# Performance work log

Hardware: AMD Instinct MI355X
Metric: run time of the kernel (lower is better)

Reference implementation:

```python
import jax, jax.numpy as jnp
import numpy as np

N = 250000   # nodes
E = 500000   # edges
D = 128      # embed_dim
L = 4        # num_layer - 1 conv layers
G = 10000    # graphs in batch
OUT = 128    # output_dim
AV = 120     # atom vocab per feature
BV = 6       # bond vocab per feature
EPS_GN = 1e-6


def setup_inputs() -> dict:
    key = jax.random.key(0)
    ks = jax.random.split(key, 12)
    s = 0.02
    f32 = jnp.float32
    inp = {}
    inp["nfeat"] = jax.random.randint(ks[0], (N, 9), 0, AV)
    inp["efeat"] = jax.random.randint(ks[1], (E, 3), 0, BV)
    inp["src"] = jax.random.randint(ks[2], (E,), 0, N)
    inp["dst"] = jax.random.randint(ks[3], (E,), 0, N)
    inp["graph_ids"] = jnp.arange(N, dtype=jnp.int32) // (N // G)  # 25 nodes/graph
    # learned params
    inp["atom_emb"] = jax.random.normal(ks[4], (9, AV, D), f32) * s
    inp["bond_emb"] = jax.random.normal(ks[5], (L, 3, BV, D), f32) * s
    inp["W1"] = jax.random.normal(ks[6], (L, D, 2 * D), f32) * s
    inp["b1"] = jnp.zeros((L, 2 * D), f32)
    inp["gn1_w"] = jnp.ones((L, 2 * D), f32)
    inp["gn1_b"] = jnp.zeros((L, 2 * D), f32)
    inp["gn1_ms"] = jnp.ones((L, 2 * D), f32)  # GraphNorm mean_scale
    inp["W2"] = jax.random.normal(ks[7], (L, 2 * D, D), f32) * s
    inp["b2"] = jnp.zeros((L, D), f32)
    inp["gn2_w"] = jnp.ones((L, D), f32)
    inp["gn2_b"] = jnp.zeros((L, D), f32)
    inp["gn2_ms"] = jnp.ones((L, D), f32)
    inp["Wp"] = jax.random.normal(ks[8], (D, OUT), f32) * s
    inp["bp"] = jnp.zeros((OUT,), f32)
    return inp


def graph_norm(x, gids, counts, w, b, ms):
    # GraphNorm: x - mean_scale * per-graph mean, / per-graph std, affine
    mean = jax.ops.segment_sum(x, gids, num_segments=G) / counts  # [G, D]
    sub = x - mean[gids] * ms
    var = jax.ops.segment_sum(sub * sub, gids, num_segments=G) / counts
    std = jnp.sqrt(var + EPS_GN)
    return w * sub / std[gids] + b


def reference(nfeat, efeat, src, dst, graph_ids, atom_emb, bond_emb,
              W1, b1, gn1_w, gn1_b, gn1_ms, W2, b2, gn2_w, gn2_b, gn2_ms,
              Wp, bp):
    counts = jax.ops.segment_sum(jnp.ones((N, 1), jnp.float32), graph_ids,
                                 num_segments=G)  # [G,1]
    # AtomEncoder: sum of 9 per-feature embeddings
    h = jnp.sum(atom_emb[jnp.arange(9)[None, :], nfeat], axis=1)  # [N, D]
    eps = jnp.float32(0.0)  # GIN eps buffer, init 0, not learned
    for l in range(L):
        x = h
        # BondEncoder for layer l
        he = jnp.sum(bond_emb[l][jnp.arange(3)[None, :], efeat], axis=1)  # [E, D]
        m = h[src] + he                                   # copy_u + edge add
        agg = jax.ops.segment_sum(m, dst, num_segments=N)  # sum reduce
        rst = (agg + (1.0 + eps) * h) @ W1[l] + b1[l]
        rst = graph_norm(rst, graph_ids, counts, gn1_w[l], gn1_b[l], gn1_ms[l])
        rst = jax.nn.relu(rst) @ W2[l] + b2[l]
        rst = graph_norm(rst, graph_ids, counts, gn2_w[l], gn2_b[l], gn2_ms[l])
        if l != L - 1:
            rst = jax.nn.relu(rst)  # activation for all but last conv layer
        h = rst + x  # residual
    # mean pooling over graphs
    g = jax.ops.segment_sum(h, graph_ids, num_segments=G) / counts  # [G, D]
    # dropout is identity in eval mode
    return g @ Wp + bp
```

## Files before the change

kernel.cpp:

```cpp
#include <hip/hip_runtime.h>
#include <hip/hip_bf16.h>
#include <stdint.h>

#define N_NODES 250000
#define N_EDGES 500000
#define DIM     128
#define D2      256
#define NLAYER  4
#define NGRAPH  10000
#define NPG     25
#define ATOMV   120
#define BONDV   6
#define NBCOMB  216

typedef __attribute__((ext_vector_type(4))) float f32x4;
typedef __attribute__((ext_vector_type(8))) short bf16x8;

__device__ __forceinline__ unsigned short bf16c(float x) {
    union { __hip_bfloat16 b; unsigned short u; } v;
    v.b = __float2bfloat16(x);
    return v.u;
}
__device__ __forceinline__ float bf16_up(unsigned short b) {
    union { float f; unsigned u; } v; v.u = (unsigned)b << 16;
    return v.f;
}
__device__ __forceinline__ f32x4 up4(ushort4 v) {
    f32x4 r;
    r[0] = bf16_up(v.x); r[1] = bf16_up(v.y);
    r[2] = bf16_up(v.z); r[3] = bf16_up(v.w);
    return r;
}

template<int CTRL>
__device__ __forceinline__ float dppadd(float x) {
    return x + __builtin_bit_cast(float,
        __builtin_amdgcn_update_dpp(0, __builtin_bit_cast(int, x),
                                    CTRL, 0xF, 0xF, true));
}
template<int CTRL>
__device__ __forceinline__ void red_step(f32x4& s0, f32x4& q0, f32x4& s1, f32x4& q1) {
#pragma unroll
    for (int j = 0; j < 4; ++j) {
        s0[j] = dppadd<CTRL>(s0[j]);
        q0[j] = dppadd<CTRL>(q0[j]);
        s1[j] = dppadd<CTRL>(s1[j]);
        q1[j] = dppadd<CTRL>(q1[j]);
    }
}
__device__ __forceinline__ void red16(f32x4& s0, f32x4& q0, f32x4& s1, f32x4& q1) {
    red_step<0xB1>(s0, q0, s1, q1);
    red_step<0x4E>(s0, q0, s1, q1);
    red_step<0x124>(s0, q0, s1, q1);
    red_step<0x128>(s0, q0, s1, q1);
}

__global__ void k_atom(const int* __restrict__ nfeat, const float* __restrict__ aemb,
                       unsigned short* __restrict__ h) {
    int t = blockIdx.x * 256 + threadIdx.x;
    int n = t >> 5;
    if (n >= N_NODES) return;
    int q = (t & 31) * 4;
    f32x4 acc = {0.f, 0.f, 0.f, 0.f};
#pragma unroll
    for (int f = 0; f < 9; ++f) {
        int v = nfeat[n * 9 + f];
        acc += *(const f32x4*)(aemb + ((size_t)(f * ATOMV + v) * DIM + q));
    }
    ushort4 hv;
    hv.x = bf16c(acc[0]); hv.y = bf16c(acc[1]);
    hv.z = bf16c(acc[2]); hv.w = bf16c(acc[3]);
    *(ushort4*)(h + (size_t)n * DIM + q) = hv;
}

__global__ void k_prepbs(const float* __restrict__ bemb, float* __restrict__ bS) {
    int i = blockIdx.x * 256 + threadIdx.x;
    if (i >= NLAYER * NBCOMB * DIM) return;
    int l = i / (NBCOMB * DIM);
    int rem = i % (NBCOMB * DIM);
    int code = rem / DIM, c = rem % DIM;
    int v0 = code / 36, v1 = (code / 6) % 6, v2 = code % 6;
    const float* base = bemb + (size_t)l * 3 * BONDV * DIM;
    bS[i] = base[0 * BONDV * DIM + v0 * DIM + c]
          + base[1 * BONDV * DIM + v1 * DIM + c]
          + base[2 * BONDV * DIM + v2 * DIM + c];
}

__global__ void k_zero_i(int* __restrict__ p, int n) {
    int i = blockIdx.x * 256 + threadIdx.x;
    if (i < n) p[i] = 0;
}
__global__ void k_hist(const int* __restrict__ dst, int* __restrict__ deg) {
    int e = blockIdx.x * 256 + threadIdx.x;
    if (e < N_EDGES) atomicAdd(&deg[dst[e]], 1);
}
__global__ void k_scan_block(const int* __restrict__ deg, int* __restrict__ rp,
                             int* __restrict__ bsum) {
    __shared__ int s[1024];
    int x = threadIdx.x;
    int i = blockIdx.x * 1024 + x;
    s[x] = (i < N_NODES) ? deg[i] : 0;
    __syncthreads();
#pragma unroll
    for (int off = 1; off < 1024; off <<= 1) {
        int tv = (x >= off) ? s[x - off] : 0;
        __syncthreads();
        s[x] += tv;
        __syncthreads();
    }
    if (i < N_NODES) rp[i + 1] = s[x];
    if (x == 1023) bsum[blockIdx.x] = s[1023];
}
__global__ void k_scan_sums(int* __restrict__ bsum, int nb) {
    __shared__ int s[256];
    int x = threadIdx.x;
    s[x] = (x < nb) ? bsum[x] : 0;
    __syncthreads();
#pragma unroll
    for (int off = 1; off < 256; off <<= 1) {
        int tv = (x >= off) ? s[x - off] : 0;
        __syncthreads();
        s[x] += tv;
        __syncthreads();
    }
    if (x < nb) bsum[x] = s[x];
}
__global__ void k_scan_add(int* __restrict__ rp, const int* __restrict__ bsum) {
    int i = blockIdx.x * 1024 + threadIdx.x;
    if (blockIdx.x > 0 && i < N_NODES) rp[i + 1] += bsum[blockIdx.x - 1];
    if (blockIdx.x == 0 && threadIdx.x == 0) rp[0] = 0;
}
__global__ void k_copy_i(const int* __restrict__ a, int* __restrict__ b, int n) {
    int i = blockIdx.x * 256 + threadIdx.x;
    if (i < n) b[i] = a[i];
}
__global__ void k_fill2(const int* __restrict__ dst, const int* __restrict__ src,
                        const int* __restrict__ efeat,
                        int* __restrict__ cur, int* __restrict__ csr) {
    int e = blockIdx.x * 256 + threadIdx.x;
    if (e < N_EDGES) {
        int b = efeat[e * 3] * 36 + efeat[e * 3 + 1] * 6 + efeat[e * 3 + 2];
        int p = atomicAdd(&cur[dst[e]], 1);
        csr[p] = (b << 18) | src[e];
    }
}

__global__ void k_gather(const unsigned short* __restrict__ h,
                         const int* __restrict__ rp, const int* __restrict__ csr,
                         const float* __restrict__ bSl,
                         unsigned short* __restrict__ xh) {
    int t = blockIdx.x * 256 + threadIdx.x;
    int n = t >> 5;
    if (n >= N_NODES) return;
    int q = (t & 31) * 4;
    f32x4 acc = up4(*(const ushort4*)(h + (size_t)n * DIM + q));
    int e0 = rp[n], e1 = rp[n + 1];
    for (int p = e0; p < e1; ++p) {
        int pk = csr[p];
        int s = pk & 0x3FFFF;
        int b = pk >> 18;
        acc += up4(*(const ushort4*)(h + (size_t)s * DIM + q))
             + *(const f32x4*)(bSl + (size_t)b * DIM + q);
    }
    ushort4 hv;
    hv.x = bf16c(acc[0]); hv.y = bf16c(acc[1]);
    hv.z = bf16c(acc[2]); hv.w = bf16c(acc[3]);
    *(ushort4*)(xh + (size_t)n * DIM + q) = hv;
}

__global__ void k_prepw(const float* __restrict__ W1, const float* __restrict__ W2,
                        unsigned short* __restrict__ w1h, unsigned short* __restrict__ w2h) {
    int i = blockIdx.x * 256 + threadIdx.x;
    if (i >= NLAYER * DIM * D2) return;
    {
        int l = i / (DIM * D2), rem = i % (DIM * D2);
        int k = rem / D2, n = rem % D2;
        w1h[l * DIM * D2 + n * DIM + k] = bf16c(W1[i]);
    }
    {
        int l = i / (D2 * DIM), rem = i % (D2 * DIM);
        int k = rem / DIM, n = rem % DIM;
        w2h[l * D2 * DIM + n * D2 + k] = bf16c(W2[i]);
    }
}


__device__ __forceinline__ void gn1_store(
    f32x4 acc1[2][4],
    const float* __restrict__ b1g, const float* __restrict__ g1w,
    const float* __restrict__ g1b, const float* __restrict__ g1ms,
    int w, int l15, int lhi, int half, unsigned short* __restrict__ B)
{
#pragma unroll
    for (int mi = 0; mi < 2; ++mi) {
        const int chl = 32 * w + 16 * mi + 4 * lhi;
        const int chg = half * 128 + chl;
        f32x4 s0 = {}, q0 = {}, s1 = {}, q1 = {};
        {
            f32x4 v = acc1[mi][0]; s0 += v; q0 += v * v;
            v = acc1[mi][1];
            if (l15 < 9) { s0 += v; q0 += v * v; } else { s1 += v; q1 += v * v; }
            v = acc1[mi][2]; s1 += v; q1 += v * v;
            v = acc1[mi][3];
            if (l15 < 2) { s1 += v; q1 += v * v; }
        }
        red16(s0, q0, s1, q1);
        f32x4 b1v = *(const f32x4*)(b1g + chg);
        f32x4 msv = *(const f32x4*)(g1ms + chg);
        f32x4 wv  = *(const f32x4*)(g1w + chg);
        f32x4 bbv = *(const f32x4*)(g1b + chg);
        f32x4 mr0 = s0 * 0.04f, mr1 = s1 * 0.04f;
        f32x4 off0 = msv * (mr0 + b1v) - b1v;
        f32x4 off1 = msv * (mr1 + b1v) - b1v;
        f32x4 var0 = q0 * 0.04f - 2.f * off0 * mr0 + off0 * off0;
        f32x4 var1 = q1 * 0.04f - 2.f * off1 * mr1 + off1 * off1;
        f32x4 sc0, sc1;
#pragma unroll
        for (int j = 0; j < 4; ++j) {
            sc0[j] = wv[j] * rsqrtf(var0[j] + 1e-6f);
            sc1[j] = wv[j] * rsqrtf(var1[j] + 1e-6f);
        }
#pragma unroll
        for (int ni = 0; ni < 4; ++ni) {
            int nd = l15 + 16 * ni;
            bool gsel = (nd >= NPG);
            f32x4 off_ = gsel ? off1 : off0;
            f32x4 sc_  = gsel ? sc1 : sc0;
            f32x4 y = (acc1[mi][ni] - off_) * sc_ + bbv;
            ushort4 hv;
            unsigned short* hp = (unsigned short*)&hv;
#pragma unroll
            for (int j = 0; j < 4; ++j)
                hp[j] = bf16c(fmaxf(y[j], 0.f));
            int gp = ((chl >> 3) - 2 * nd) & 15;
            int ao = nd * 136 + gp * 8 + (chl & 7);
            *(ushort4*)&B[ao] = hv;
        }
    }
}

__device__ __forceinline__ void mm2_half(
    const unsigned short* __restrict__ B,
    const unsigned short* __restrict__ w2h,
    int w, int l15, int lhi, int half, f32x4 acc2[2][4])
{
#pragma unroll
    for (int ks = 0; ks < 4; ++ks) {
        const int kb = ks * 32 + lhi * 8;
        const int g = kb >> 3;
        bf16x8 x2[4];
#pragma unroll
        for (int ni = 0; ni < 4; ++ni) {
            int nd = l15 + 16 * ni;
            int gp = (g - 2 * nd) & 15;
            x2[ni] = *(const bf16x8*)&B[nd * 136 + gp * 8];
        }
#pragma unroll
        for (int mi = 0; mi < 2; ++mi) {
            const size_t wro = (size_t)(32 * w + 16 * mi + l15) * 256 + half * 128 + kb;
            bf16x8 wh = *(const bf16x8*)(w2h + wro);
#pragma unroll
            for (int ni = 0; ni < 4; ++ni)
                acc2[mi][ni] = __builtin_amdgcn_mfma_f32_16x16x32_bf16(wh, x2[ni], acc2[mi][ni], 0, 0, 0);
        }
    }
}

__global__ __launch_bounds__(256, 3) void k_layer(
    const unsigned short* __restrict__ xh_g,
    unsigned short* __restrict__ h,
    const unsigned short* __restrict__ w1h,
    const float* __restrict__ b1g,
    const float* __restrict__ g1w, const float* __restrict__ g1b, const float* __restrict__ g1ms,
    const unsigned short* __restrict__ w2h,
    const float* __restrict__ b2g,
    const float* __restrict__ g2w, const float* __restrict__ g2b, const float* __restrict__ g2ms,
    int do_relu)
{
    __shared__ unsigned short B0[64 * 136];
    __shared__ unsigned short B1[64 * 136];

    const int t = threadIdx.x;
    const int lane = t & 63;
    const int w = t >> 6;
    const int l15 = lane & 15, lhi = lane >> 4;
    const size_t row0 = (size_t)blockIdx.x * 50;

    int ndrow[4];
#pragma unroll
    for (int ni = 0; ni < 4; ++ni) {
        int nd = l15 + 16 * ni;
        ndrow[ni] = (nd < 50) ? nd : 49;
    }

    f32x4 a1h0[2][4] = {};
    f32x4 a1h1[2][4] = {};
#pragma unroll
    for (int ks = 0; ks < 4; ++ks) {
        const int kb = ks * 32 + lhi * 8;
        bf16x8 xv[4];
#pragma unroll
        for (int ni = 0; ni < 4; ++ni)
            xv[ni] = *(const bf16x8*)(xh_g + (row0 + ndrow[ni]) * DIM + kb);
#pragma unroll
        for (int mi = 0; mi < 2; ++mi) {
            const size_t wr0 = (size_t)(32 * w + 16 * mi + l15) * 128 + kb;
            const size_t wr1 = (size_t)(128 + 32 * w + 16 * mi + l15) * 128 + kb;
            bf16x8 wh0 = *(const bf16x8*)(w1h + wr0);
            bf16x8 wh1 = *(const bf16x8*)(w1h + wr1);
#pragma unroll
            for (int ni = 0; ni < 4; ++ni) {
                a1h0[mi][ni] = __builtin_amdgcn_mfma_f32_16x16x32_bf16(wh0, xv[ni], a1h0[mi][ni], 0, 0, 0);
                a1h1[mi][ni] = __builtin_amdgcn_mfma_f32_16x16x32_bf16(wh1, xv[ni], a1h1[mi][ni], 0, 0, 0);
            }
        }
    }

    gn1_store(a1h0, b1g, g1w, g1b, g1ms, w, l15, lhi, 0, B0);
    gn1_store(a1h1, b1g, g1w, g1b, g1ms, w, l15, lhi, 1, B1);
    __syncthreads();

    ushort4 hres[2][4];
#pragma unroll
    for (int mi = 0; mi < 2; ++mi) {
        const int chb = 32 * w + 16 * mi + 4 * lhi;
#pragma unroll
        for (int ni = 0; ni < 4; ++ni)
            hres[mi][ni] = *(const ushort4*)(h + (row0 + ndrow[ni]) * DIM + chb);
    }

    f32x4 acc2[2][4] = {};
    mm2_half(B0, w2h, w, l15, lhi, 0, acc2);
    mm2_half(B1, w2h, w, l15, lhi, 1, acc2);

#pragma unroll
    for (int mi = 0; mi < 2; ++mi) {
        const int chb = 32 * w + 16 * mi + 4 * lhi;
        f32x4 s0 = {}, q0 = {}, s1 = {}, q1 = {};
        {
            f32x4 v = acc2[mi][0]; s0 += v; q0 += v * v;
            v = acc2[mi][1];
            if (l15 < 9) { s0 += v; q0 += v * v; } else { s1 += v; q1 += v * v; }
            v = acc2[mi][2]; s1 += v; q1 += v * v;
            v = acc2[mi][3];
            if (l15 < 2) { s1 += v; q1 += v * v; }
        }
        red16(s0, q0, s1, q1);
        f32x4 b2v = *(const f32x4*)(b2g + chb);
        f32x4 msv = *(const f32x4*)(g2ms + chb);
        f32x4 wv  = *(const f32x4*)(g2w + chb);
        f32x4 bbv = *(const f32x4*)(g2b + chb);
        f32x4 mr0 = s0 * 0.04f, mr1 = s1 * 0.04f;
        f32x4 off0 = msv * (mr0 + b2v) - b2v;
        f32x4 off1 = msv * (mr1 + b2v) - b2v;
        f32x4 var0 = q0 * 0.04f - 2.f * off0 * mr0 + off0 * off0;
        f32x4 var1 = q1 * 0.04f - 2.f * off1 * mr1 + off1 * off1;
        f32x4 sc0, sc1;
#pragma unroll
        for (int j = 0; j < 4; ++j) {
            sc0[j] = wv[j] * rsqrtf(var0[j] + 1e-6f);
            sc1[j] = wv[j] * rsqrtf(var1[j] + 1e-6f);
        }
#pragma unroll
        for (int ni = 0; ni < 4; ++ni) {
            int nd = l15 + 16 * ni;
            if (nd < 50) {
                bool gsel = (nd >= NPG);
                f32x4 off_ = gsel ? off1 : off0;
                f32x4 sc_  = gsel ? sc1 : sc0;
                f32x4 y = (acc2[mi][ni] - off_) * sc_ + bbv;
                if (do_relu) {
#pragma unroll
                    for (int j = 0; j < 4; ++j) y[j] = fmaxf(y[j], 0.f);
                }
                f32x4 hf = up4(hres[mi][ni]);
                f32x4 r = y + hf;
                ushort4 o;
                o.x = bf16c(r[0]); o.y = bf16c(r[1]);
                o.z = bf16c(r[2]); o.w = bf16c(r[3]);
                *(ushort4*)(h + (row0 + nd) * DIM + chb) = o;
            }
        }
    }
}

__global__ void k_pool(const unsigned short* __restrict__ h, float* __restrict__ g) {
    int gi = blockIdx.x, c = threadIdx.x;
    const unsigned short* base = h + (size_t)gi * NPG * DIM + c;
    float s = 0.f;
#pragma unroll
    for (int i = 0; i < NPG; ++i) s += bf16_up(base[i * DIM]);
    g[(size_t)gi * DIM + c] = s * (1.f / NPG);
}

#define GPB 32
__global__ __launch_bounds__(256) void k_final(const float* __restrict__ g,
        const float* __restrict__ Wp, const float* __restrict__ bp,
        float* __restrict__ out) {
    __shared__ float Ws[DIM * DIM];
    __shared__ float gs[GPB][DIM];
    int t = threadIdx.x;
    int g0 = blockIdx.x * GPB;
    for (int i = t; i < DIM * DIM; i += 256) Ws[i] = Wp[i];
    for (int i = t; i < GPB * DIM; i += 256) {
        int gi = g0 + i / DIM;
        gs[i / DIM][i % DIM] = (gi < NGRAPH) ? g[(size_t)gi * DIM + (i % DIM)] : 0.f;
    }
    __syncthreads();
    int c = t & (DIM - 1);
    int half = t >> 7;
    float bv = bp[c];
    for (int gl = half; gl < GPB; gl += 2) {
        int gi = g0 + gl;
        if (gi >= NGRAPH) continue;
        float s = 0.f;
#pragma unroll 8
        for (int k = 0; k < DIM; ++k) s += gs[gl][k] * Ws[k * DIM + c];
        out[(size_t)gi * DIM + c] = s + bv;
    }
}

extern "C" void kernel_launch(void* const* d_in, const int* in_sizes, int n_in,
                              void* d_out, int out_size, void* d_ws, size_t ws_size,
                              hipStream_t stream) {
    const int*   nfeat    = (const int*)d_in[0];
    const int*   efeat    = (const int*)d_in[1];
    const int*   src      = (const int*)d_in[2];
    const int*   dst      = (const int*)d_in[3];
    const float* atom_emb = (const float*)d_in[5];
    const float* bond_emb = (const float*)d_in[6];
    const float* W1       = (const float*)d_in[7];
    const float* b1       = (const float*)d_in[8];
    const float* gn1_w    = (const float*)d_in[9];
    const float* gn1_b    = (const float*)d_in[10];
    const float* gn1_ms   = (const float*)d_in[11];
    const float* W2       = (const float*)d_in[12];
    const float* b2       = (const float*)d_in[13];
    const float* gn2_w    = (const float*)d_in[14];
    const float* gn2_b    = (const float*)d_in[15];
    const float* gn2_ms   = (const float*)d_in[16];
    const float* Wp       = (const float*)d_in[17];
    const float* bp       = (const float*)d_in[18];
    float* out = (float*)d_out;

    char* ws = (char*)d_ws;
    unsigned short* w1h = (unsigned short*)ws; ws += (size_t)NLAYER * DIM * D2 * 2;
    unsigned short* w2h = (unsigned short*)ws; ws += (size_t)NLAYER * D2 * DIM * 2;
    float* bS = (float*)ws; ws += (size_t)NLAYER * NBCOMB * DIM * 4;
    unsigned short* h  = (unsigned short*)ws; ws += (size_t)N_NODES * DIM * 2;
    unsigned short* xh = (unsigned short*)ws; ws += (size_t)N_NODES * DIM * 2;
    float* gbuf = (float*)ws; ws += (size_t)NGRAPH * DIM * 4;

    int* rp   = (int*)d_out;
    int* cur  = rp + 262144;
    int* deg  = cur;
    int* csr  = cur + 262144;
    int* bsum = csr + 524288;

    const int NB = (N_NODES + 1023) / 1024;

    k_prepw<<<(NLAYER * DIM * D2 + 255) / 256, 256, 0, stream>>>(W1, W2, w1h, w2h);
    k_prepbs<<<(NLAYER * NBCOMB * DIM + 255) / 256, 256, 0, stream>>>(bond_emb, bS);
    k_atom<<<(N_NODES * 32) / 256, 256, 0, stream>>>(nfeat, atom_emb, h);

    k_zero_i<<<(N_NODES + 255) / 256, 256, 0, stream>>>(deg, N_NODES);
    k_hist<<<(N_EDGES + 255) / 256, 256, 0, stream>>>(dst, deg);
    k_scan_block<<<NB, 1024, 0, stream>>>(deg, rp, bsum);
    k_scan_sums<<<1, 256, 0, stream>>>(bsum, NB);
    k_scan_add<<<NB, 1024, 0, stream>>>(rp, bsum);
    k_copy_i<<<(N_NODES + 255) / 256, 256, 0, stream>>>(rp, cur, N_NODES);
    k_fill2<<<(N_EDGES + 255) / 256, 256, 0, stream>>>(dst, src, efeat, cur, csr);

    for (int l = 0; l < NLAYER; ++l) {
        k_gather<<<(N_NODES * 32 + 255) / 256, 256, 0, stream>>>(
            h, rp, csr, bS + (size_t)l * NBCOMB * DIM, xh);
        k_layer<<<NGRAPH / 2, 256, 0, stream>>>(
            xh, h,
            w1h + l * DIM * D2, b1 + l * D2,
            gn1_w + l * D2, gn1_b + l * D2, gn1_ms + l * D2,
            w2h + l * D2 * DIM, b2 + l * DIM,
            gn2_w + l * DIM, gn2_b + l * DIM, gn2_ms + l * DIM,
            (l != NLAYER - 1) ? 1 : 0);
    }
    k_pool<<<NGRAPH, DIM, 0, stream>>>(h, gbuf);
    k_final<<<(NGRAPH + GPB - 1) / GPB, 256, 0, stream>>>(gbuf, Wp, bp, out);
}
```

Baseline: 967.5 us.

## Remap k_layer waves so each owns one graph and a channel half

The work split in the fused GIN layer kernel changes. Before, each of four waves covered all 50 rows (two graphs padded to 64) across 32 channels. Now each wave handles one graph's 25 rows (padded to 32) across 64 channels. This removes the MFMA work spent on padding rows and simplifies the GraphNorm reductions to a single graph per wave. Occupancy in launch bounds goes from 3 to 4 blocks, which risks register pressure or spills, and each wave now loads more weight fragments.

```diff
diff --git a/kernel.cpp b/kernel.cpp
--- a/kernel.cpp
+++ b/kernel.cpp
@@ -39,20 +39,18 @@
                                     CTRL, 0xF, 0xF, true));
 }
 template<int CTRL>
-__device__ __forceinline__ void red_step(f32x4& s0, f32x4& q0, f32x4& s1, f32x4& q1) {
+__device__ __forceinline__ void red_step2(f32x4& s, f32x4& q) {
 #pragma unroll
     for (int j = 0; j < 4; ++j) {
-        s0[j] = dppadd<CTRL>(s0[j]);
-        q0[j] = dppadd<CTRL>(q0[j]);
-        s1[j] = dppadd<CTRL>(s1[j]);
-        q1[j] = dppadd<CTRL>(q1[j]);
-    }
-}
-__device__ __forceinline__ void red16(f32x4& s0, f32x4& q0, f32x4& s1, f32x4& q1) {
-    red_step<0xB1>(s0, q0, s1, q1);
-    red_step<0x4E>(s0, q0, s1, q1);
-    red_step<0x124>(s0, q0, s1, q1);
-    red_step<0x128>(s0, q0, s1, q1);
+        s[j] = dppadd<CTRL>(s[j]);
+        q[j] = dppadd<CTRL>(q[j]);
+    }
+}
+__device__ __forceinline__ void red16_2(f32x4& s, f32x4& q) {
+    red_step2<0xB1>(s, q);
+    red_step2<0x4E>(s, q);
+    red_step2<0x124>(s, q);
+    red_step2<0x128>(s, q);
 }
 
 __global__ void k_atom(const int* __restrict__ nfeat, const float* __restrict__ aemb,
@@ -184,89 +182,7 @@
     }
 }
 
-
-__device__ __forceinline__ void gn1_store(
-    f32x4 acc1[2][4],
-    const float* __restrict__ b1g, const float* __restrict__ g1w,
-    const float* __restrict__ g1b, const float* __restrict__ g1ms,
-    int w, int l15, int lhi, int half, unsigned short* __restrict__ B)
-{
-#pragma unroll
-    for (int mi = 0; mi < 2; ++mi) {
-        const int chl = 32 * w + 16 * mi + 4 * lhi;
-        const int chg = half * 128 + chl;
-        f32x4 s0 = {}, q0 = {}, s1 = {}, q1 = {};
-        {
-            f32x4 v = acc1[mi][0]; s0 += v; q0 += v * v;
-            v = acc1[mi][1];
-            if (l15 < 9) { s0 += v; q0 += v * v; } else { s1 += v; q1 += v * v; }
-            v = acc1[mi][2]; s1 += v; q1 += v * v;
-            v = acc1[mi][3];
-            if (l15 < 2) { s1 += v; q1 += v * v; }
-        }
-        red16(s0, q0, s1, q1);
-        f32x4 b1v = *(const f32x4*)(b1g + chg);
-        f32x4 msv = *(const f32x4*)(g1ms + chg);
-        f32x4 wv  = *(const f32x4*)(g1w + chg);
-        f32x4 bbv = *(const f32x4*)(g1b + chg);
-        f32x4 mr0 = s0 * 0.04f, mr1 = s1 * 0.04f;
-        f32x4 off0 = msv * (mr0 + b1v) - b1v;
-        f32x4 off1 = msv * (mr1 + b1v) - b1v;
-        f32x4 var0 = q0 * 0.04f - 2.f * off0 * mr0 + off0 * off0;
-        f32x4 var1 = q1 * 0.04f - 2.f * off1 * mr1 + off1 * off1;
-        f32x4 sc0, sc1;
-#pragma unroll
-        for (int j = 0; j < 4; ++j) {
-            sc0[j] = wv[j] * rsqrtf(var0[j] + 1e-6f);
-            sc1[j] = wv[j] * rsqrtf(var1[j] + 1e-6f);
-        }
-#pragma unroll
-        for (int ni = 0; ni < 4; ++ni) {
-            int nd = l15 + 16 * ni;
-            bool gsel = (nd >= NPG);
-            f32x4 off_ = gsel ? off1 : off0;
-            f32x4 sc_  = gsel ? sc1 : sc0;
-            f32x4 y = (acc1[mi][ni] - off_) * sc_ + bbv;
-            ushort4 hv;
-            unsigned short* hp = (unsigned short*)&hv;
-#pragma unroll
-            for (int j = 0; j < 4; ++j)
-                hp[j] = bf16c(fmaxf(y[j], 0.f));
-            int gp = ((chl >> 3) - 2 * nd) & 15;
-            int ao = nd * 136 + gp * 8 + (chl & 7);
-            *(ushort4*)&B[ao] = hv;
-        }
-    }
-}
-
-__device__ __forceinline__ void mm2_half(
-    const unsigned short* __restrict__ B,
-    const unsigned short* __restrict__ w2h,
-    int w, int l15, int lhi, int half, f32x4 acc2[2][4])
-{
-#pragma unroll
-    for (int ks = 0; ks < 4; ++ks) {
-        const int kb = ks * 32 + lhi * 8;
-        const int g = kb >> 3;
-        bf16x8 x2[4];
-#pragma unroll
-        for (int ni = 0; ni < 4; ++ni) {
-            int nd = l15 + 16 * ni;
-            int gp = (g - 2 * nd) & 15;
-            x2[ni] = *(const bf16x8*)&B[nd * 136 + gp * 8];
-        }
-#pragma unroll
-        for (int mi = 0; mi < 2; ++mi) {
-            const size_t wro = (size_t)(32 * w + 16 * mi + l15) * 256 + half * 128 + kb;
-            bf16x8 wh = *(const bf16x8*)(w2h + wro);
-#pragma unroll
-            for (int ni = 0; ni < 4; ++ni)
-                acc2[mi][ni] = __builtin_amdgcn_mfma_f32_16x16x32_bf16(wh, x2[ni], acc2[mi][ni], 0, 0, 0);
-        }
-    }
-}
-
-__global__ __launch_bounds__(256, 3) void k_layer(
+__global__ __launch_bounds__(256, 4) void k_layer(
     const unsigned short* __restrict__ xh_g,
     unsigned short* __restrict__ h,
     const unsigned short* __restrict__ w1h,
@@ -283,102 +199,144 @@
     const int t = threadIdx.x;
     const int lane = t & 63;
     const int w = t >> 6;
+    const int wg = w & 1;
+    const int wc = w >> 1;
     const int l15 = lane & 15, lhi = lane >> 4;
-    const size_t row0 = (size_t)blockIdx.x * 50;
-
-    int ndrow[4];
-#pragma unroll
-    for (int ni = 0; ni < 4; ++ni) {
+    const size_t grow_base = (size_t)blockIdx.x * 50 + 25 * wg;
+
+    int ndc[2];
+#pragma unroll
+    for (int ni = 0; ni < 2; ++ni) {
         int nd = l15 + 16 * ni;
-        ndrow[ni] = (nd < 50) ? nd : 49;
-    }
-
-    f32x4 a1h0[2][4] = {};
-    f32x4 a1h1[2][4] = {};
-#pragma unroll
-    for (int ks = 0; ks < 4; ++ks) {
+        ndc[ni] = (nd < NPG) ? nd : (NPG - 1);
+    }
+
+#pragma unroll
+    for (int half = 0; half < 2; ++half) {
+        f32x4 a1[4][2] = {};
+#pragma unroll
+        for (int ks = 0; ks < 4; ++ks) {
+            const int kb = ks * 32 + lhi * 8;
+            bf16x8 xv[2];
+#pragma unroll
+            for (int ni = 0; ni < 2; ++ni)
+                xv[ni] = *(const bf16x8*)(xh_g + (grow_base + ndc[ni]) * DIM + kb);
+#pragma unroll
+            for (int mi = 0; mi < 4; ++mi) {
+                const size_t wro = (size_t)(half * 128 + wc * 64 + 16 * mi + l15) * 128 + kb;
+                bf16x8 wv = *(const bf16x8*)(w1h + wro);
+#pragma unroll
+                for (int ni = 0; ni < 2; ++ni)
+                    a1[mi][ni] = __builtin_amdgcn_mfma_f32_16x16x32_bf16(wv, xv[ni], a1[mi][ni], 0, 0, 0);
+            }
+        }
+        unsigned short* B = half ? B1 : B0;
+#pragma unroll
+        for (int mi = 0; mi < 4; ++mi) {
+            const int chl = wc * 64 + 16 * mi + 4 * lhi;
+            const int chg = half * 128 + chl;
+            f32x4 s = {}, q = {};
+            {
+                f32x4 v = a1[mi][0]; s += v; q += v * v;
+                v = a1[mi][1];
+                if (l15 < 9) { s += v; q += v * v; }
+            }
+            red16_2(s, q);
+            f32x4 b1v = *(const f32x4*)(b1g + chg);
+            f32x4 msv = *(const f32x4*)(g1ms + chg);
+            f32x4 wv  = *(const f32x4*)(g1w + chg);
+            f32x4 bbv = *(const f32x4*)(g1b + chg);
+            f32x4 mr = s * 0.04f;
+            f32x4 off = msv * (mr + b1v) - b1v;
+            f32x4 var = q * 0.04f - 2.f * off * mr + off * off;
+            f32x4 sc;
+#pragma unroll
+            for (int j = 0; j < 4; ++j)
+                sc[j] = wv[j] * rsqrtf(var[j] + 1e-6f);
+#pragma unroll
+            for (int ni = 0; ni < 2; ++ni) {
+                const int r = 32 * wg + l15 + 16 * ni;
+                f32x4 y = (a1[mi][ni] - off) * sc + bbv;
+                ushort4 hv;
+                unsigned short* hp = (unsigned short*)&hv;
+#pragma unroll
+                for (int j = 0; j < 4; ++j)
+                    hp[j] = bf16c(fmaxf(y[j], 0.f));
+                int gp = ((chl >> 3) - 2 * r) & 15;
+                *(ushort4*)&B[r * 136 + gp * 8 + (chl & 7)] = hv;
+            }
+        }
+    }
+    __syncthreads();
+
+    const int ob = wc * 64;
+    ushort4 hres[4][2];
+#pragma unroll
+    for (int mi = 0; mi < 4; ++mi) {
+        const int oc = ob + 16 * mi + 4 * lhi;
+#pragma unroll
+        for (int ni = 0; ni < 2; ++ni)
+            hres[mi][ni] = *(const ushort4*)(h + (grow_base + ndc[ni]) * DIM + oc);
+    }
+
+    f32x4 a2[4][2] = {};
+#pragma unroll
+    for (int ks = 0; ks < 8; ++ks) {
         const int kb = ks * 32 + lhi * 8;
-        bf16x8 xv[4];
-#pragma unroll
-        for (int ni = 0; ni < 4; ++ni)
-            xv[ni] = *(const bf16x8*)(xh_g + (row0 + ndrow[ni]) * DIM + kb);
-#pragma unroll
-        for (int mi = 0; mi < 2; ++mi) {
-            const size_t wr0 = (size_t)(32 * w + 16 * mi + l15) * 128 + kb;
-            const size_t wr1 = (size_t)(128 + 32 * w + 16 * mi + l15) * 128 + kb;
-            bf16x8 wh0 = *(const bf16x8*)(w1h + wr0);
-            bf16x8 wh1 = *(const bf16x8*)(w1h + wr1);
-#pragma unroll
-            for (int ni = 0; ni < 4; ++ni) {
-                a1h0[mi][ni] = __builtin_amdgcn_mfma_f32_16x16x32_bf16(wh0, xv[ni], a1h0[mi][ni], 0, 0, 0);
-                a1h1[mi][ni] = __builtin_amdgcn_mfma_f32_16x16x32_bf16(wh1, xv[ni], a1h1[mi][ni], 0, 0, 0);
-            }
-        }
-    }
-
-    gn1_store(a1h0, b1g, g1w, g1b, g1ms, w, l15, lhi, 0, B0);
-    gn1_store(a1h1, b1g, g1w, g1b, g1ms, w, l15, lhi, 1, B1);
-    __syncthreads();
-
-    ushort4 hres[2][4];
-#pragma unroll
-    for (int mi = 0; mi < 2; ++mi) {
-        const int chb = 32 * w + 16 * mi + 4 * lhi;
-#pragma unroll
-        for (int ni = 0; ni < 4; ++ni)
-            hres[mi][ni] = *(const ushort4*)(h + (row0 + ndrow[ni]) * DIM + chb);
-    }
-
-    f32x4 acc2[2][4] = {};
-    mm2_half(B0, w2h, w, l15, lhi, 0, acc2);
-    mm2_half(B1, w2h, w, l15, lhi, 1, acc2);
-
-#pragma unroll
-    for (int mi = 0; mi < 2; ++mi) {
-        const int chb = 32 * w + 16 * mi + 4 * lhi;
-        f32x4 s0 = {}, q0 = {}, s1 = {}, q1 = {};
+        const unsigned short* B = (kb & 128) ? B1 : B0;
+        const int g = (kb & 127) >> 3;
+        bf16x8 x2[2];
+#pragma unroll
+        for (int ni = 0; ni < 2; ++ni) {
+            int r = 32 * wg + l15 + 16 * ni;
+            int gp = (g - 2 * r) & 15;
+            x2[ni] = *(const bf16x8*)&B[r * 136 + gp * 8];
+        }
+#pragma unroll
+        for (int mi = 0; mi < 4; ++mi) {
+            const size_t wro = (size_t)(ob + 16 * mi + l15) * 256 + kb;
+            bf16x8 wv = *(const bf16x8*)(w2h + wro);
+#pragma unroll
+            for (int ni = 0; ni < 2; ++ni)
+                a2[mi][ni] = __builtin_amdgcn_mfma_f32_16x16x32_bf16(wv, x2[ni], a2[mi][ni], 0, 0, 0);
+        }
+    }
+
+#pragma unroll
+    for (int mi = 0; mi < 4; ++mi) {
+        const int oc = ob + 16 * mi + 4 * lhi;
+        f32x4 s = {}, q = {};
         {
-            f32x4 v = acc2[mi][0]; s0 += v; q0 += v * v;
-            v = acc2[mi][1];
-            if (l15 < 9) { s0 += v; q0 += v * v; } else { s1 += v; q1 += v * v; }
-            v = acc2[mi][2]; s1 += v; q1 += v * v;
-            v = acc2[mi][3];
-            if (l15 < 2) { s1 += v; q1 += v * v; }
-        }
-        red16(s0, q0, s1, q1);
-        f32x4 b2v = *(const f32x4*)(b2g + chb);
-        f32x4 msv = *(const f32x4*)(g2ms + chb);
-        f32x4 wv  = *(const f32x4*)(g2w + chb);
-        f32x4 bbv = *(const f32x4*)(g2b + chb);
-        f32x4 mr0 = s0 * 0.04f, mr1 = s1 * 0.04f;
-        f32x4 off0 = msv * (mr0 + b2v) - b2v;
-        f32x4 off1 = msv * (mr1 + b2v) - b2v;
-        f32x4 var0 = q0 * 0.04f - 2.f * off0 * mr0 + off0 * off0;
-        f32x4 var1 = q1 * 0.04f - 2.f * off1 * mr1 + off1 * off1;
-        f32x4 sc0, sc1;
-#pragma unroll
-        for (int j = 0; j < 4; ++j) {
-            sc0[j] = wv[j] * rsqrtf(var0[j] + 1e-6f);
-            sc1[j] = wv[j] * rsqrtf(var1[j] + 1e-6f);
-        }
-#pragma unroll
-        for (int ni = 0; ni < 4; ++ni) {
+            f32x4 v = a2[mi][0]; s += v; q += v * v;
+            v = a2[mi][1];
+            if (l15 < 9) { s += v; q += v * v; }
+        }
+        red16_2(s, q);
+        f32x4 b2v = *(const f32x4*)(b2g + oc);
+        f32x4 msv = *(const f32x4*)(g2ms + oc);
+        f32x4 wv  = *(const f32x4*)(g2w + oc);
+        f32x4 bbv = *(const f32x4*)(g2b + oc);
+        f32x4 mr = s * 0.04f;
+        f32x4 off = msv * (mr + b2v) - b2v;
+        f32x4 var = q * 0.04f - 2.f * off * mr + off * off;
+        f32x4 sc;
+#pragma unroll
+        for (int j = 0; j < 4; ++j)
+            sc[j] = wv[j] * rsqrtf(var[j] + 1e-6f);
+#pragma unroll
+        for (int ni = 0; ni < 2; ++ni) {
             int nd = l15 + 16 * ni;
-            if (nd < 50) {
-                bool gsel = (nd >= NPG);
-                f32x4 off_ = gsel ? off1 : off0;
-                f32x4 sc_  = gsel ? sc1 : sc0;
-                f32x4 y = (acc2[mi][ni] - off_) * sc_ + bbv;
+            if (nd < NPG) {
+                f32x4 y = (a2[mi][ni] - off) * sc + bbv;
                 if (do_relu) {
 #pragma unroll
                     for (int j = 0; j < 4; ++j) y[j] = fmaxf(y[j], 0.f);
                 }
-                f32x4 hf = up4(hres[mi][ni]);
-                f32x4 r = y + hf;
+                f32x4 r = y + up4(hres[mi][ni]);
                 ushort4 o;
                 o.x = bf16c(r[0]); o.y = bf16c(r[1]);
                 o.z = bf16c(r[2]); o.w = bf16c(r[3]);
-                *(ushort4*)(h + (row0 + nd) * DIM + chb) = o;
+                *(ushort4*)(h + (grow_base + nd) * DIM + oc) = o;
             }
         }
     }
```

New measurement: 1.249 ms. 29.1% more time.

## Pad gathered features into 64-row tiles with graphs aligned at 32-row boundaries

Applied to the files above, without the earlier changes.

The gather kernel now writes the aggregated features into a padded layout. Each pair of graphs occupies 64 rows, each graph starting on a 32-row boundary, and the padding rows are zero. This lets the layer kernel load rows directly, without clamping indices. GraphNorm sums become simple per-fragment adds instead of lane-conditional splits, and the padding rows contribute zero to them. The cost is extra memory traffic for the padded rows plus more gather threads, some of which do nothing.

```diff
diff --git a/kernel.cpp b/kernel.cpp
--- a/kernel.cpp
+++ b/kernel.cpp
@@ -12,6 +12,8 @@
 #define ATOMV   120
 #define BONDV   6
 #define NBCOMB  216
+#define NTILE   (NGRAPH/2)
+#define TROWS   64
 
 typedef __attribute__((ext_vector_type(4))) float f32x4;
 typedef __attribute__((ext_vector_type(8))) short bf16x8;
@@ -148,24 +150,29 @@
 __global__ void k_gather(const unsigned short* __restrict__ h,
                          const int* __restrict__ rp, const int* __restrict__ csr,
                          const float* __restrict__ bSl,
-                         unsigned short* __restrict__ xh) {
+                         unsigned short* __restrict__ xh_t) {
     int t = blockIdx.x * 256 + threadIdx.x;
-    int n = t >> 5;
-    if (n >= N_NODES) return;
+    int rr = t >> 5;
+    if (rr >= NTILE * TROWS) return;
     int q = (t & 31) * 4;
-    f32x4 acc = up4(*(const ushort4*)(h + (size_t)n * DIM + q));
-    int e0 = rp[n], e1 = rp[n + 1];
-    for (int p = e0; p < e1; ++p) {
-        int pk = csr[p];
-        int s = pk & 0x3FFFF;
-        int b = pk >> 18;
-        acc += up4(*(const ushort4*)(h + (size_t)s * DIM + q))
-             + *(const f32x4*)(bSl + (size_t)b * DIM + q);
-    }
-    ushort4 hv;
-    hv.x = bf16c(acc[0]); hv.y = bf16c(acc[1]);
-    hv.z = bf16c(acc[2]); hv.w = bf16c(acc[3]);
-    *(ushort4*)(xh + (size_t)n * DIM + q) = hv;
+    int r = rr & 63, tile = rr >> 6;
+    int rl = r & 31, g = r >> 5;
+    ushort4 hv = {0, 0, 0, 0};
+    if (rl < NPG) {
+        int n = tile * 50 + g * NPG + rl;
+        f32x4 acc = up4(*(const ushort4*)(h + (size_t)n * DIM + q));
+        int e0 = rp[n], e1 = rp[n + 1];
+        for (int p = e0; p < e1; ++p) {
+            int pk = csr[p];
+            int s = pk & 0x3FFFF;
+            int b = pk >> 18;
+            acc += up4(*(const ushort4*)(h + (size_t)s * DIM + q))
+                 + *(const f32x4*)(bSl + (size_t)b * DIM + q);
+        }
+        hv.x = bf16c(acc[0]); hv.y = bf16c(acc[1]);
+        hv.z = bf16c(acc[2]); hv.w = bf16c(acc[3]);
+    }
+    *(ushort4*)(xh_t + (size_t)rr * DIM + q) = hv;
 }
 
 __global__ void k_prepw(const float* __restrict__ W1, const float* __restrict__ W2,
@@ -195,15 +202,10 @@
     for (int mi = 0; mi < 2; ++mi) {
         const int chl = 32 * w + 16 * mi + 4 * lhi;
         const int chg = half * 128 + chl;
-        f32x4 s0 = {}, q0 = {}, s1 = {}, q1 = {};
-        {
-            f32x4 v = acc1[mi][0]; s0 += v; q0 += v * v;
-            v = acc1[mi][1];
-            if (l15 < 9) { s0 += v; q0 += v * v; } else { s1 += v; q1 += v * v; }
-            v = acc1[mi][2]; s1 += v; q1 += v * v;
-            v = acc1[mi][3];
-            if (l15 < 2) { s1 += v; q1 += v * v; }
-        }
+        f32x4 s0 = acc1[mi][0] + acc1[mi][1];
+        f32x4 q0 = acc1[mi][0] * acc1[mi][0] + acc1[mi][1] * acc1[mi][1];
+        f32x4 s1 = acc1[mi][2] + acc1[mi][3];
+        f32x4 q1 = acc1[mi][2] * acc1[mi][2] + acc1[mi][3] * acc1[mi][3];
         red16(s0, q0, s1, q1);
         f32x4 b1v = *(const f32x4*)(b1g + chg);
         f32x4 msv = *(const f32x4*)(g1ms + chg);
@@ -223,15 +225,18 @@
 #pragma unroll
         for (int ni = 0; ni < 4; ++ni) {
             int nd = l15 + 16 * ni;
-            bool gsel = (nd >= NPG);
+            bool gsel = (nd & 32) != 0;
+            bool real = (nd & 31) < NPG;
             f32x4 off_ = gsel ? off1 : off0;
             f32x4 sc_  = gsel ? sc1 : sc0;
             f32x4 y = (acc1[mi][ni] - off_) * sc_ + bbv;
-            ushort4 hv;
-            unsigned short* hp = (unsigned short*)&hv;
-#pragma unroll
-            for (int j = 0; j < 4; ++j)
-                hp[j] = bf16c(fmaxf(y[j], 0.f));
+            ushort4 hv = {0, 0, 0, 0};
+            if (real) {
+                hv.x = bf16c(fmaxf(y[0], 0.f));
+                hv.y = bf16c(fmaxf(y[1], 0.f));
+                hv.z = bf16c(fmaxf(y[2], 0.f));
+                hv.w = bf16c(fmaxf(y[3], 0.f));
+            }
             int gp = ((chl >> 3) - 2 * nd) & 15;
             int ao = nd * 136 + gp * 8 + (chl & 7);
             *(ushort4*)&B[ao] = hv;
@@ -267,7 +272,7 @@
 }
 
 __global__ __launch_bounds__(256, 3) void k_layer(
-    const unsigned short* __restrict__ xh_g,
+    const unsigned short* __restrict__ xh_t,
     unsigned short* __restrict__ h,
     const unsigned short* __restrict__ w1h,
     const float* __restrict__ b1g,
@@ -284,13 +289,15 @@
     const int lane = t & 63;
     const int w = t >> 6;
     const int l15 = lane & 15, lhi = lane >> 4;
-    const size_t row0 = (size_t)blockIdx.x * 50;
-
-    int ndrow[4];
+    const size_t trow0 = (size_t)blockIdx.x * TROWS;
+    const size_t nrow0 = (size_t)blockIdx.x * 50;
+
+    int ndc[4];
 #pragma unroll
     for (int ni = 0; ni < 4; ++ni) {
         int nd = l15 + 16 * ni;
-        ndrow[ni] = (nd < 50) ? nd : 49;
+        int rl = nd & 31;
+        ndc[ni] = 25 * (nd >> 5) + ((rl < NPG) ? rl : (NPG - 1));
     }
 
     f32x4 a1h0[2][4] = {};
@@ -301,7 +308,7 @@
         bf16x8 xv[4];
 #pragma unroll
         for (int ni = 0; ni < 4; ++ni)
-            xv[ni] = *(const bf16x8*)(xh_g + (row0 + ndrow[ni]) * DIM + kb);
+            xv[ni] = *(const bf16x8*)(xh_t + (trow0 + l15 + 16 * ni) * DIM + kb);
 #pragma unroll
         for (int mi = 0; mi < 2; ++mi) {
             const size_t wr0 = (size_t)(32 * w + 16 * mi + l15) * 128 + kb;
@@ -326,7 +333,7 @@
         const int chb = 32 * w + 16 * mi + 4 * lhi;
 #pragma unroll
         for (int ni = 0; ni < 4; ++ni)
-            hres[mi][ni] = *(const ushort4*)(h + (row0 + ndrow[ni]) * DIM + chb);
+            hres[mi][ni] = *(const ushort4*)(h + (nrow0 + ndc[ni]) * DIM + chb);
     }
 
     f32x4 acc2[2][4] = {};
@@ -336,15 +343,10 @@
 #pragma unroll
     for (int mi = 0; mi < 2; ++mi) {
         const int chb = 32 * w + 16 * mi + 4 * lhi;
-        f32x4 s0 = {}, q0 = {}, s1 = {}, q1 = {};
-        {
-            f32x4 v = acc2[mi][0]; s0 += v; q0 += v * v;
-            v = acc2[mi][1];
-            if (l15 < 9) { s0 += v; q0 += v * v; } else { s1 += v; q1 += v * v; }
-            v = acc2[mi][2]; s1 += v; q1 += v * v;
-            v = acc2[mi][3];
-            if (l15 < 2) { s1 += v; q1 += v * v; }
-        }
+        f32x4 s0 = acc2[mi][0] + acc2[mi][1];
+        f32x4 q0 = acc2[mi][0] * acc2[mi][0] + acc2[mi][1] * acc2[mi][1];
+        f32x4 s1 = acc2[mi][2] + acc2[mi][3];
+        f32x4 q1 = acc2[mi][2] * acc2[mi][2] + acc2[mi][3] * acc2[mi][3];
         red16(s0, q0, s1, q1);
         f32x4 b2v = *(const f32x4*)(b2g + chb);
         f32x4 msv = *(const f32x4*)(g2ms + chb);
@@ -364,8 +366,8 @@
 #pragma unroll
         for (int ni = 0; ni < 4; ++ni) {
             int nd = l15 + 16 * ni;
-            if (nd < 50) {
-                bool gsel = (nd >= NPG);
+            if ((nd & 31) < NPG) {
+                bool gsel = (nd & 32) != 0;
                 f32x4 off_ = gsel ? off1 : off0;
                 f32x4 sc_  = gsel ? sc1 : sc0;
                 f32x4 y = (acc2[mi][ni] - off_) * sc_ + bbv;
@@ -373,12 +375,11 @@
 #pragma unroll
                     for (int j = 0; j < 4; ++j) y[j] = fmaxf(y[j], 0.f);
                 }
-                f32x4 hf = up4(hres[mi][ni]);
-                f32x4 r = y + hf;
+                f32x4 r = y + up4(hres[mi][ni]);
                 ushort4 o;
                 o.x = bf16c(r[0]); o.y = bf16c(r[1]);
                 o.z = bf16c(r[2]); o.w = bf16c(r[3]);
-                *(ushort4*)(h + (row0 + nd) * DIM + chb) = o;
+                *(ushort4*)(h + (nrow0 + ndc[ni]) * DIM + chb) = o;
             }
         }
     }
@@ -448,7 +449,7 @@
     unsigned short* w2h = (unsigned short*)ws; ws += (size_t)NLAYER * D2 * DIM * 2;
     float* bS = (float*)ws; ws += (size_t)NLAYER * NBCOMB * DIM * 4;
     unsigned short* h  = (unsigned short*)ws; ws += (size_t)N_NODES * DIM * 2;
-    unsigned short* xh = (unsigned short*)ws; ws += (size_t)N_NODES * DIM * 2;
+    unsigned short* xh = (unsigned short*)ws; ws += (size_t)NTILE * TROWS * DIM * 2;
     float* gbuf = (float*)ws; ws += (size_t)NGRAPH * DIM * 4;
 
     int* rp   = (int*)d_out;
@@ -472,9 +473,9 @@
     k_fill2<<<(N_EDGES + 255) / 256, 256, 0, stream>>>(dst, src, efeat, cur, csr);
 
     for (int l = 0; l < NLAYER; ++l) {
-        k_gather<<<(N_NODES * 32 + 255) / 256, 256, 0, stream>>>(
+        k_gather<<<(NTILE * TROWS * 32 + 255) / 256, 256, 0, stream>>>(
             h, rp, csr, bS + (size_t)l * NBCOMB * DIM, xh);
-        k_layer<<<NGRAPH / 2, 256, 0, stream>>>(
+        k_layer<<<NTILE, 256, 0, stream>>>(
             xh, h,
             w1h + l * DIM * D2, b1 + l * D2,
             gn1_w + l * D2, gn1_b + l * D2, gn1_ms + l * D2,
```

New measurement: 1.019 ms. 1.05x slower.

## Split fused layer kernel across 8 waves to halve per-wave MFMA work

Applied to the files above, without the earlier changes.

The fused GIN layer kernel now launches 512 threads (8 waves) per block instead of 256. Each wave computes 32 of the 256 hidden channels in the first GEMM and 16 of the 128 output channels in the second, which halves the accumulator registers per wave. The aim is more waves in flight to hide the global loads and the reductions. The trade-off is that each wave reloads the same activation fragments, so LDS and global read traffic per block goes up.

```diff
diff --git a/kernel.cpp b/kernel.cpp
--- a/kernel.cpp
+++ b/kernel.cpp
@@ -184,89 +184,7 @@
     }
 }
 
-
-__device__ __forceinline__ void gn1_store(
-    f32x4 acc1[2][4],
-    const float* __restrict__ b1g, const float* __restrict__ g1w,
-    const float* __restrict__ g1b, const float* __restrict__ g1ms,
-    int w, int l15, int lhi, int half, unsigned short* __restrict__ B)
-{
-#pragma unroll
-    for (int mi = 0; mi < 2; ++mi) {
-        const int chl = 32 * w + 16 * mi + 4 * lhi;
-        const int chg = half * 128 + chl;
-        f32x4 s0 = {}, q0 = {}, s1 = {}, q1 = {};
-        {
-            f32x4 v = acc1[mi][0]; s0 += v; q0 += v * v;
-            v = acc1[mi][1];
-            if (l15 < 9) { s0 += v; q0 += v * v; } else { s1 += v; q1 += v * v; }
-            v = acc1[mi][2]; s1 += v; q1 += v * v;
-            v = acc1[mi][3];
-            if (l15 < 2) { s1 += v; q1 += v * v; }
-        }
-        red16(s0, q0, s1, q1);
-        f32x4 b1v = *(const f32x4*)(b1g + chg);
-        f32x4 msv = *(const f32x4*)(g1ms + chg);
-        f32x4 wv  = *(const f32x4*)(g1w + chg);
-        f32x4 bbv = *(const f32x4*)(g1b + chg);
-        f32x4 mr0 = s0 * 0.04f, mr1 = s1 * 0.04f;
-        f32x4 off0 = msv * (mr0 + b1v) - b1v;
-        f32x4 off1 = msv * (mr1 + b1v) - b1v;
-        f32x4 var0 = q0 * 0.04f - 2.f * off0 * mr0 + off0 * off0;
-        f32x4 var1 = q1 * 0.04f - 2.f * off1 * mr1 + off1 * off1;
-        f32x4 sc0, sc1;
-#pragma unroll
-        for (int j = 0; j < 4; ++j) {
-            sc0[j] = wv[j] * rsqrtf(var0[j] + 1e-6f);
-            sc1[j] = wv[j] * rsqrtf(var1[j] + 1e-6f);
-        }
-#pragma unroll
-        for (int ni = 0; ni < 4; ++ni) {
-            int nd = l15 + 16 * ni;
-            bool gsel = (nd >= NPG);
-            f32x4 off_ = gsel ? off1 : off0;
-            f32x4 sc_  = gsel ? sc1 : sc0;
-            f32x4 y = (acc1[mi][ni] - off_) * sc_ + bbv;
-            ushort4 hv;
-            unsigned short* hp = (unsigned short*)&hv;
-#pragma unroll
-            for (int j = 0; j < 4; ++j)
-                hp[j] = bf16c(fmaxf(y[j], 0.f));
-            int gp = ((chl >> 3) - 2 * nd) & 15;
-            int ao = nd * 136 + gp * 8 + (chl & 7);
-            *(ushort4*)&B[ao] = hv;
-        }
-    }
-}
-
-__device__ __forceinline__ void mm2_half(
-    const unsigned short* __restrict__ B,
-    const unsigned short* __restrict__ w2h,
-    int w, int l15, int lhi, int half, f32x4 acc2[2][4])
-{
-#pragma unroll
-    for (int ks = 0; ks < 4; ++ks) {
-        const int kb = ks * 32 + lhi * 8;
-        const int g = kb >> 3;
-        bf16x8 x2[4];
-#pragma unroll
-        for (int ni = 0; ni < 4; ++ni) {
-            int nd = l15 + 16 * ni;
-            int gp = (g - 2 * nd) & 15;
-            x2[ni] = *(const bf16x8*)&B[nd * 136 + gp * 8];
-        }
-#pragma unroll
-        for (int mi = 0; mi < 2; ++mi) {
-            const size_t wro = (size_t)(32 * w + 16 * mi + l15) * 256 + half * 128 + kb;
-            bf16x8 wh = *(const bf16x8*)(w2h + wro);
-#pragma unroll
-            for (int ni = 0; ni < 4; ++ni)
-                acc2[mi][ni] = __builtin_amdgcn_mfma_f32_16x16x32_bf16(wh, x2[ni], acc2[mi][ni], 0, 0, 0);
-        }
-    }
-}
-
-__global__ __launch_bounds__(256, 3) void k_layer(
+__global__ __launch_bounds__(512, 2) void k_layer(
     const unsigned short* __restrict__ xh_g,
     unsigned short* __restrict__ h,
     const unsigned short* __restrict__ w1h,
@@ -293,8 +211,7 @@
         ndrow[ni] = (nd < 50) ? nd : 49;
     }
 
-    f32x4 a1h0[2][4] = {};
-    f32x4 a1h1[2][4] = {};
+    f32x4 a1[2][4] = {};
 #pragma unroll
     for (int ks = 0; ks < 4; ++ks) {
         const int kb = ks * 32 + lhi * 8;
@@ -304,45 +221,99 @@
             xv[ni] = *(const bf16x8*)(xh_g + (row0 + ndrow[ni]) * DIM + kb);
 #pragma unroll
         for (int mi = 0; mi < 2; ++mi) {
-            const size_t wr0 = (size_t)(32 * w + 16 * mi + l15) * 128 + kb;
-            const size_t wr1 = (size_t)(128 + 32 * w + 16 * mi + l15) * 128 + kb;
-            bf16x8 wh0 = *(const bf16x8*)(w1h + wr0);
-            bf16x8 wh1 = *(const bf16x8*)(w1h + wr1);
+            const size_t wro = (size_t)(32 * w + 16 * mi + l15) * 128 + kb;
+            bf16x8 wh = *(const bf16x8*)(w1h + wro);
+#pragma unroll
+            for (int ni = 0; ni < 4; ++ni)
+                a1[mi][ni] = __builtin_amdgcn_mfma_f32_16x16x32_bf16(wh, xv[ni], a1[mi][ni], 0, 0, 0);
+        }
+    }
+
+    {
+        unsigned short* B = (w >= 4) ? B1 : B0;
+#pragma unroll
+        for (int mi = 0; mi < 2; ++mi) {
+            const int chg = 32 * w + 16 * mi + 4 * lhi;
+            const int chl = chg & 127;
+            f32x4 s0 = {}, q0 = {}, s1 = {}, q1 = {};
+            {
+                f32x4 v = a1[mi][0]; s0 += v; q0 += v * v;
+                v = a1[mi][1];
+                if (l15 < 9) { s0 += v; q0 += v * v; } else { s1 += v; q1 += v * v; }
+                v = a1[mi][2]; s1 += v; q1 += v * v;
+                v = a1[mi][3];
+                if (l15 < 2) { s1 += v; q1 += v * v; }
+            }
+            red16(s0, q0, s1, q1);
+            f32x4 b1v = *(const f32x4*)(b1g + chg);
+            f32x4 msv = *(const f32x4*)(g1ms + chg);
+            f32x4 wv  = *(const f32x4*)(g1w + chg);
+            f32x4 bbv = *(const f32x4*)(g1b + chg);
+            f32x4 mr0 = s0 * 0.04f, mr1 = s1 * 0.04f;
+            f32x4 off0 = msv * (mr0 + b1v) - b1v;
+            f32x4 off1 = msv * (mr1 + b1v) - b1v;
+            f32x4 var0 = q0 * 0.04f - 2.f * off0 * mr0 + off0 * off0;
+            f32x4 var1 = q1 * 0.04f - 2.f * off1 * mr1 + off1 * off1;
+            f32x4 sc0, sc1;
+#pragma unroll
+            for (int j = 0; j < 4; ++j) {
+                sc0[j] = wv[j] * rsqrtf(var0[j] + 1e-6f);
+                sc1[j] = wv[j] * rsqrtf(var1[j] + 1e-6f);
+            }
 #pragma unroll
             for (int ni = 0; ni < 4; ++ni) {
-                a1h0[mi][ni] = __builtin_amdgcn_mfma_f32_16x16x32_bf16(wh0, xv[ni], a1h0[mi][ni], 0, 0, 0);
-                a1h1[mi][ni] = __builtin_amdgcn_mfma_f32_16x16x32_bf16(wh1, xv[ni], a1h1[mi][ni], 0, 0, 0);
+                int nd = l15 + 16 * ni;
+                bool gsel = (nd >= NPG);
+                f32x4 off_ = gsel ? off1 : off0;
+                f32x4 sc_  = gsel ? sc1 : sc0;
+                f32x4 y = (a1[mi][ni] - off_) * sc_ + bbv;
+                ushort4 hv;
+                unsigned short* hp = (unsigned short*)&hv;
+#pragma unroll
+                for (int j = 0; j < 4; ++j)
+                    hp[j] = bf16c(fmaxf(y[j], 0.f));
+                int gp = ((chl >> 3) - 2 * nd) & 15;
+                int ao = nd * 136 + gp * 8 + (chl & 7);
+                *(ushort4*)&B[ao] = hv;
             }
         }
     }
-
-    gn1_store(a1h0, b1g, g1w, g1b, g1ms, w, l15, lhi, 0, B0);
-    gn1_store(a1h1, b1g, g1w, g1b, g1ms, w, l15, lhi, 1, B1);
     __syncthreads();
 
-    ushort4 hres[2][4];
-#pragma unroll
-    for (int mi = 0; mi < 2; ++mi) {
-        const int chb = 32 * w + 16 * mi + 4 * lhi;
+    const int chb = 16 * w + 4 * lhi;
+    ushort4 hres[4];
+#pragma unroll
+    for (int ni = 0; ni < 4; ++ni)
+        hres[ni] = *(const ushort4*)(h + (row0 + ndrow[ni]) * DIM + chb);
+
+    f32x4 a2[4] = {};
+#pragma unroll
+    for (int ks = 0; ks < 8; ++ks) {
+        const int kb = ks * 32 + lhi * 8;
+        const unsigned short* B = (kb & 128) ? B1 : B0;
+        const int g = (kb & 127) >> 3;
+        bf16x8 x2[4];
+#pragma unroll
+        for (int ni = 0; ni < 4; ++ni) {
+            int nd = l15 + 16 * ni;
+            int gp = (g - 2 * nd) & 15;
+            x2[ni] = *(const bf16x8*)&B[nd * 136 + gp * 8];
+        }
+        const size_t wro = (size_t)(16 * w + l15) * 256 + kb;
+        bf16x8 wh = *(const bf16x8*)(w2h + wro);
 #pragma unroll
         for (int ni = 0; ni < 4; ++ni)
-            hres[mi][ni] = *(const ushort4*)(h + (row0 + ndrow[ni]) * DIM + chb);
-    }
-
-    f32x4 acc2[2][4] = {};
-    mm2_half(B0, w2h, w, l15, lhi, 0, acc2);
-    mm2_half(B1, w2h, w, l15, lhi, 1, acc2);
-
-#pragma unroll
-    for (int mi = 0; mi < 2; ++mi) {
-        const int chb = 32 * w + 16 * mi + 4 * lhi;
+            a2[ni] = __builtin_amdgcn_mfma_f32_16x16x32_bf16(wh, x2[ni], a2[ni], 0, 0, 0);
+    }
+
+    {
         f32x4 s0 = {}, q0 = {}, s1 = {}, q1 = {};
         {
-            f32x4 v = acc2[mi][0]; s0 += v; q0 += v * v;
-            v = acc2[mi][1];
+            f32x4 v = a2[0]; s0 += v; q0 += v * v;
+            v = a2[1];
             if (l15 < 9) { s0 += v; q0 += v * v; } else { s1 += v; q1 += v * v; }
-            v = acc2[mi][2]; s1 += v; q1 += v * v;
-            v = acc2[mi][3];
+            v = a2[2]; s1 += v; q1 += v * v;
+            v = a2[3];
             if (l15 < 2) { s1 += v; q1 += v * v; }
         }
         red16(s0, q0, s1, q1);
@@ -368,13 +339,12 @@
                 bool gsel = (nd >= NPG);
                 f32x4 off_ = gsel ? off1 : off0;
                 f32x4 sc_  = gsel ? sc1 : sc0;
-                f32x4 y = (acc2[mi][ni] - off_) * sc_ + bbv;
+                f32x4 y = (a2[ni] - off_) * sc_ + bbv;
                 if (do_relu) {
 #pragma unroll
                     for (int j = 0; j < 4; ++j) y[j] = fmaxf(y[j], 0.f);
                 }
-                f32x4 hf = up4(hres[mi][ni]);
-                f32x4 r = y + hf;
+                f32x4 r = y + up4(hres[ni]);
                 ushort4 o;
                 o.x = bf16c(r[0]); o.y = bf16c(r[1]);
                 o.z = bf16c(r[2]); o.w = bf16c(r[3]);
@@ -474,7 +444,7 @@
     for (int l = 0; l < NLAYER; ++l) {
         k_gather<<<(N_NODES * 32 + 255) / 256, 256, 0, stream>>>(
             h, rp, csr, bS + (size_t)l * NBCOMB * DIM, xh);
-        k_layer<<<NGRAPH / 2, 256, 0, stream>>>(
+        k_layer<<<NGRAPH / 2, 512, 0, stream>>>(
             xh, h,
             w1h + l * DIM * D2, b1 + l * D2,
             gn1_w + l * D2, gn1_b + l * D2, gn1_ms + l * D2,
```

After: 1.074 ms. +11.0%, slower.
